# Optimization experiments

Measured on AMD Instinct MI355X. Metric: run time of the kernel, lower is better.

## Reference

```python
import jax, jax.numpy as jnp
import numpy as np


def setup_inputs() -> dict:
    key = jax.random.key(0)
    k1, k2 = jax.random.split(key)
    x1 = jax.random.normal(k1, (8192, 256), dtype=jnp.float32)
    x2 = jax.random.normal(k2, (8192, 256), dtype=jnp.float32)
    return {"x1": x1, "x2": x2}


def reference(x1, x2):
    # Euclidean distance matrix, equivalent to torch.cdist(x1, x2, p=2.0).
    # GEMM-based expansion: ||a-b||^2 = ||a||^2 + ||b||^2 - 2 a.b
    sq1 = jnp.sum(x1 * x1, axis=-1, keepdims=True)          # [N, 1]
    sq2 = jnp.sum(x2 * x2, axis=-1, keepdims=True)          # [M, 1]
    cross = jnp.einsum('nd,md->nm', x1, x2)                 # [N, M]
    d2 = sq1 + sq2.T - 2.0 * cross
    d2 = jnp.maximum(d2, 0.0)  # guard tiny negatives from cancellation
    return jnp.sqrt(d2)
```

## Files before the change

kernel.cpp:

```cpp
#include <hip/hip_runtime.h>


typedef __bf16 v8bf __attribute__((ext_vector_type(8)));
typedef float v4f __attribute__((ext_vector_type(4)));

#define NROWS 8192
#define KDIM  256
#define TILE  128
#define BK    64
#define NTHREADS 512

typedef const __attribute__((address_space(1))) ushort* gas_ushort_p;
typedef __attribute__((address_space(3))) ushort* las_ushort_p;

__device__ __forceinline__ void async_load16(const ushort* g, ushort* l) {
    __builtin_amdgcn_global_load_lds((gas_ushort_p)g, (las_ushort_p)l, 16, 0, 0);
}

__device__ __forceinline__ ushort f2bf_rne(float f) {
    union { float f; unsigned u; } a; a.f = f;
    unsigned u = a.u + 0x7fffu + ((a.u >> 16) & 1u);
    return (ushort)(u >> 16);
}

__global__ __launch_bounds__(256) void cvt_norm_kernel(
    const float* __restrict__ x1, const float* __restrict__ x2,
    ushort* __restrict__ xb1, ushort* __restrict__ xb2,
    float* __restrict__ sq1, float* __restrict__ sq2) {
    const int half2 = NROWS / 4;
    const float* x = (blockIdx.x < half2) ? x1 : x2;
    ushort* xb     = (blockIdx.x < half2) ? xb1 : xb2;
    float* sq      = (blockIdx.x < half2) ? sq1 : sq2;
    const int bb   = (blockIdx.x < half2) ? blockIdx.x : blockIdx.x - half2;

    const int wave = threadIdx.x >> 6;
    const int lane = threadIdx.x & 63;
    const int row  = bb * 4 + wave;
    const float4 v = ((const float4*)(x + (size_t)row * KDIM))[lane];
    float s = v.x * v.x + v.y * v.y + v.z * v.z + v.w * v.w;
#pragma unroll
    for (int off = 32; off; off >>= 1) s += __shfl_down(s, off);
    if (lane == 0) sq[row] = s;
    ushort4 o;
    o.x = f2bf_rne(v.x); o.y = f2bf_rne(v.y);
    o.z = f2bf_rne(v.z); o.w = f2bf_rne(v.w);
    ((ushort4*)(xb + (size_t)row * KDIM))[lane] = o;
}

__global__ __launch_bounds__(NTHREADS, 6) void cdist_mfma_kernel(
    const ushort* __restrict__ A,
    const ushort* __restrict__ B,
    const float* __restrict__ sq1,
    const float* __restrict__ sq2,
    float* __restrict__ out) {
    __shared__ ushort As[TILE * BK];
    __shared__ ushort Bs[TILE * BK];

    const int bid = blockIdx.x;
    const int xcd = bid & 7;
    const int cc  = bid >> 3;
    const int bm  = ((xcd & 3) << 4) | (cc & 15);
    const int bn  = ((xcd >> 2) << 5) | (cc >> 4);

    const int tid  = threadIdx.x;
    const int wave = tid >> 6;
    const int lane = tid & 63;
    const int wr = wave >> 2;
    const int wc = wave & 3;

    const int lrow = lane >> 3;
    const int lk   = (lane & 7) * 8;

    v4f acc[4][2];
#pragma unroll
    for (int i = 0; i < 4; ++i)
#pragma unroll
        for (int j = 0; j < 2; ++j) acc[i][j] = (v4f){0.f, 0.f, 0.f, 0.f};

    const int half = lane >> 4;
    const int mrow = lane & 15;

    for (int kt = 0; kt < KDIM; kt += BK) {
        __syncthreads();
#pragma unroll
        for (int c = 0; c < 2; ++c) {
            const int rbase = wave * 16 + c * 8;
            const ushort* ga =
                A + (size_t)(bm * TILE + rbase + lrow) * KDIM + kt + lk;
            const ushort* gb =
                B + (size_t)(bn * TILE + rbase + lrow) * KDIM + kt + lk;
            async_load16(ga, &As[rbase * BK]);
            async_load16(gb, &Bs[rbase * BK]);
        }
        __syncthreads();
#pragma unroll
        for (int kk = 0; kk < BK; kk += 32) {
            v8bf a[4], b[2];
#pragma unroll
            for (int i = 0; i < 4; ++i)
                a[i] = *(const v8bf*)&As[(wr * 64 + i * 16 + mrow) * BK + kk + half * 8];
#pragma unroll
            for (int j = 0; j < 2; ++j)
                b[j] = *(const v8bf*)&Bs[(wc * 32 + j * 16 + mrow) * BK + kk + half * 8];
#pragma unroll
            for (int i = 0; i < 4; ++i)
#pragma unroll
                for (int j = 0; j < 2; ++j)
                    acc[i][j] = __builtin_amdgcn_mfma_f32_16x16x32_bf16(
                        a[i], b[j], acc[i][j], 0, 0, 0);
        }
    }

    const int m0 = bm * TILE + wr * 64;
    const int n0 = bn * TILE + wc * 32;
    float s2v[2];
#pragma unroll
    for (int j = 0; j < 2; ++j) s2v[j] = sq2[n0 + j * 16 + mrow];
#pragma unroll
    for (int i = 0; i < 4; ++i) {
        const int rbase = m0 + i * 16 + half * 4;
        float s1v[4];
#pragma unroll
        for (int r = 0; r < 4; ++r) s1v[r] = sq1[rbase + r];
#pragma unroll
        for (int r = 0; r < 4; ++r) {
            float* op = out + (size_t)(rbase + r) * NROWS + n0 + mrow;
#pragma unroll
            for (int j = 0; j < 2; ++j) {
                const float d2 = s1v[r] + s2v[j] - 2.0f * acc[i][j][r];
                op[j * 16] = sqrtf(fmaxf(d2, 0.0f));
            }
        }
    }
}

extern "C" void kernel_launch(void* const* d_in, const int* in_sizes, int n_in,
                              void* d_out, int out_size, void* d_ws, size_t ws_size,
                              hipStream_t stream) {
    const float* x1 = (const float*)d_in[0];
    const float* x2 = (const float*)d_in[1];
    float* out = (float*)d_out;

    ushort* Ab = (ushort*)d_ws;
    ushort* Bb = Ab + (size_t)NROWS * KDIM;
    float* sq1 = (float*)(Bb + (size_t)NROWS * KDIM);
    float* sq2 = sq1 + NROWS;

    cvt_norm_kernel<<<NROWS / 2, 256, 0, stream>>>(x1, x2, Ab, Bb, sq1, sq2);

    cdist_mfma_kernel<<<4096, NTHREADS, 0, stream>>>(Ab, Bb, sq1, sq2, out);
}
```

Baseline: 314.7 us.

## Make cdist GEMM persistent with double-buffered LDS and XOR-swizzled layout

Launches 512 persistent blocks that each loop over 8 output tiles instead of 4096 one-tile blocks. LDS is double-buffered so the async global->LDS load of the next K-slice (or next tile) overlaps the MFMA work on the current one. The LDS layout is XOR-swizzled to avoid bank conflicts on fragment reads. Occupancy drops (launch bounds go from 6 to 4) and the epilogue stores now sit inside the pipelined loop, so output writes may no longer overlap well across blocks.

```diff
diff --git a/kernel.cpp b/kernel.cpp
--- a/kernel.cpp
+++ b/kernel.cpp
@@ -9,6 +9,8 @@
 #define TILE  128
 #define BK    64
 #define NTHREADS 512
+#define NTILES  8
+#define NSTEPS  (NTILES * 4)
 
 typedef const __attribute__((address_space(1))) ushort* gas_ushort_p;
 typedef __attribute__((address_space(3))) ushort* las_ushort_p;
@@ -47,29 +49,32 @@
     ((ushort4*)(xb + (size_t)row * KDIM))[lane] = o;
 }
 
-__global__ __launch_bounds__(NTHREADS, 6) void cdist_mfma_kernel(
+__global__ __launch_bounds__(NTHREADS, 4) void cdist_mfma_kernel(
     const ushort* __restrict__ A,
     const ushort* __restrict__ B,
     const float* __restrict__ sq1,
     const float* __restrict__ sq2,
     float* __restrict__ out) {
-    __shared__ ushort As[TILE * BK];
-    __shared__ ushort Bs[TILE * BK];
+    __shared__ ushort As[2][TILE * BK];
+    __shared__ ushort Bs[2][TILE * BK];
 
     const int bid = blockIdx.x;
     const int xcd = bid & 7;
-    const int cc  = bid >> 3;
-    const int bm  = ((xcd & 3) << 4) | (cc & 15);
-    const int bn  = ((xcd >> 2) << 5) | (cc >> 4);
+    const int lb  = bid >> 3;
 
     const int tid  = threadIdx.x;
     const int wave = tid >> 6;
     const int lane = tid & 63;
     const int wr = wave >> 2;
     const int wc = wave & 3;
+    const int half = lane >> 4;
+    const int mrow = lane & 15;
 
     const int lrow = lane >> 3;
-    const int lk   = (lane & 7) * 8;
+    const int lcol = ((lane & 7) ^ lrow) * 8;
+
+    const int swzlo = (half ^ (mrow & 7)) * 8;
+    const int swzhi = ((half + 4) ^ (mrow & 7)) * 8;
 
     v4f acc[4][2];
 #pragma unroll
@@ -77,31 +82,46 @@
 #pragma unroll
         for (int j = 0; j < 2; ++j) acc[i][j] = (v4f){0.f, 0.f, 0.f, 0.f};
 
-    const int half = lane >> 4;
-    const int mrow = lane & 15;
+    auto tileRows = [&](int t, int& rA, int& rB) {
+        const int ct = lb + (t << 6);
+        rA = (((xcd & 3) << 4) | (ct & 15)) * TILE;
+        rB = (((xcd >> 2) << 5) | (ct >> 4)) * TILE;
+    };
 
-    for (int kt = 0; kt < KDIM; kt += BK) {
-        __syncthreads();
+    auto stage = [&](int buf, int rA, int rB, int kt) {
 #pragma unroll
         for (int c = 0; c < 2; ++c) {
             const int rbase = wave * 16 + c * 8;
-            const ushort* ga =
-                A + (size_t)(bm * TILE + rbase + lrow) * KDIM + kt + lk;
-            const ushort* gb =
-                B + (size_t)(bn * TILE + rbase + lrow) * KDIM + kt + lk;
-            async_load16(ga, &As[rbase * BK]);
-            async_load16(gb, &Bs[rbase * BK]);
+            async_load16(A + (size_t)(rA + rbase + lrow) * KDIM + kt + lcol,
+                         &As[buf][rbase * BK]);
+            async_load16(B + (size_t)(rB + rbase + lrow) * KDIM + kt + lcol,
+                         &Bs[buf][rbase * BK]);
         }
-        __syncthreads();
+    };
+
+    int rA, rB, nA, nB;
+    tileRows(0, rA, rB);
+    stage(0, rA, rB, 0);
+    __syncthreads();
+    nA = rA; nB = rB;
+    int buf = 0;
+
+#pragma unroll 4
+    for (int s = 0; s < NSTEPS; ++s) {
+        if (s + 1 < NSTEPS) {
+            if (((s + 1) & 3) == 0) tileRows((s + 1) >> 2, nA, nB);
+            stage(buf ^ 1, nA, nB, ((s + 1) & 3) * BK);
+        }
 #pragma unroll
         for (int kk = 0; kk < BK; kk += 32) {
+            const int swz = kk ? swzhi : swzlo;
             v8bf a[4], b[2];
 #pragma unroll
             for (int i = 0; i < 4; ++i)
-                a[i] = *(const v8bf*)&As[(wr * 64 + i * 16 + mrow) * BK + kk + half * 8];
+                a[i] = *(const v8bf*)&As[buf][(wr * 64 + i * 16 + mrow) * BK + swz];
 #pragma unroll
             for (int j = 0; j < 2; ++j)
-                b[j] = *(const v8bf*)&Bs[(wc * 32 + j * 16 + mrow) * BK + kk + half * 8];
+                b[j] = *(const v8bf*)&Bs[buf][(wc * 32 + j * 16 + mrow) * BK + swz];
 #pragma unroll
             for (int i = 0; i < 4; ++i)
 #pragma unroll
@@ -109,27 +129,30 @@
                     acc[i][j] = __builtin_amdgcn_mfma_f32_16x16x32_bf16(
                         a[i], b[j], acc[i][j], 0, 0, 0);
         }
-    }
-
-    const int m0 = bm * TILE + wr * 64;
-    const int n0 = bn * TILE + wc * 32;
-    float s2v[2];
+        __syncthreads();
+        buf ^= 1;
+        if ((s & 3) == 3) {
+            const int m0 = rA + wr * 64;
+            const int n0 = rB + wc * 32;
+            float s2v[2];
 #pragma unroll
-    for (int j = 0; j < 2; ++j) s2v[j] = sq2[n0 + j * 16 + mrow];
+            for (int j = 0; j < 2; ++j) s2v[j] = sq2[n0 + j * 16 + mrow];
 #pragma unroll
-    for (int i = 0; i < 4; ++i) {
-        const int rbase = m0 + i * 16 + half * 4;
-        float s1v[4];
+            for (int i = 0; i < 4; ++i) {
+                const int rbase = m0 + i * 16 + half * 4;
 #pragma unroll
-        for (int r = 0; r < 4; ++r) s1v[r] = sq1[rbase + r];
+                for (int r = 0; r < 4; ++r) {
+                    const float s1 = sq1[rbase + r];
+                    float* op = out + (size_t)(rbase + r) * NROWS + n0 + mrow;
 #pragma unroll
-        for (int r = 0; r < 4; ++r) {
-            float* op = out + (size_t)(rbase + r) * NROWS + n0 + mrow;
-#pragma unroll
-            for (int j = 0; j < 2; ++j) {
-                const float d2 = s1v[r] + s2v[j] - 2.0f * acc[i][j][r];
-                op[j * 16] = sqrtf(fmaxf(d2, 0.0f));
+                    for (int j = 0; j < 2; ++j) {
+                        const float d2 = s1 + s2v[j] - 2.0f * acc[i][j][r];
+                        op[j * 16] = sqrtf(fmaxf(d2, 0.0f));
+                        acc[i][j][r] = 0.f;
+                    }
+                }
             }
+            rA = nA; rB = nB;
         }
     }
 }
@@ -148,5 +171,5 @@
 
     cvt_norm_kernel<<<NROWS / 2, 256, 0, stream>>>(x1, x2, Ab, Bb, sq1, sq2);
 
-    cdist_mfma_kernel<<<4096, NTHREADS, 0, stream>>>(Ab, Bb, sq1, sq2, out);
+    cdist_mfma_kernel<<<512, NTHREADS, 0, stream>>>(Ab, Bb, sq1, sq2, out);
 }
```

Result: slower. 345.9 us (+9.9%).
